# Kernel optimization log

Hardware: AMD Instinct MI355X
Metric: run time of the kernel (lower is better)

## Reference

```python
import jax, jax.numpy as jnp
import numpy as np

BUFFER_C = 1.25

def setup_inputs() -> dict:
    key = jax.random.key(0)
    k1, k2, k3 = jax.random.split(key, 3)
    T, D, E = 4096, 1024, 8
    x = jax.random.normal(k1, (T, D), dtype=jnp.float32)
    Wg = jax.random.normal(k2, (D, E), dtype=jnp.float32) / np.sqrt(D)
    bg = jnp.zeros((E,), dtype=jnp.float32)
    W = jax.random.normal(k3, (E, D, D), dtype=jnp.float32) / np.sqrt(D)
    b = jnp.zeros((E, D), dtype=jnp.float32)
    return {"x": x, "Wg": Wg, "bg": bg, "W": W, "b": b}


def reference(x, Wg, bg, W, b):
    # Top-1 (Switch-style) routing with capacity buffer, per-expert Linear,
    # prob-weighted combine, plus load-balancing aux loss.
    T, D = x.shape
    E = W.shape[0]
    capacity = int(BUFFER_C * T / E)

    logits = x @ Wg + bg                      # [T, E]
    probs = jax.nn.softmax(logits, axis=-1)   # [T, E]
    top_idx = jnp.argmax(probs, axis=-1)      # [T]
    top_prob = jnp.take_along_axis(probs, top_idx[:, None], axis=-1)[:, 0]

    onehot = jax.nn.one_hot(top_idx, E, dtype=x.dtype)       # [T, E]
    # 1-indexed position of each token within its expert's buffer
    pos = jnp.cumsum(onehot, axis=0) * onehot                # [T, E]
    dispatch = jnp.where((onehot > 0) & (pos <= capacity), 1.0, 0.0).astype(x.dtype)

    # dense dispatch/combine equivalent of the masked per-expert loop
    xe = jnp.einsum('te,td->etd', dispatch, x)               # [E, T, D]
    ye = jnp.einsum('etd,edf->etf', xe, W) + b[:, None, :]   # [E, T, D]
    y = jnp.einsum('te,etf->tf', dispatch, ye)               # [T, D] (0 for dropped)
    out = y * top_prob[:, None]

    # aux load-balance loss: E * sum_e f_e * P_e
    f = onehot.mean(axis=0)
    P = probs.mean(axis=0)
    aux_loss = E * jnp.sum(f * P)
    return out, aux_loss
```

## Files before the change

### kernel.cpp

```cpp
#include <hip/hip_runtime.h>
#include <hip/hip_bf16.h>
#include <cstdint>

#define T_TOK 4096
#define D_DIM 1024
#define E_EXP 8
#define CAP   640
#define MAXDROP 3456
#define MT    10
#define GBLK  1024

typedef __attribute__((ext_vector_type(8))) short short8;
typedef __attribute__((ext_vector_type(4))) float f32x4;

__device__ inline unsigned short f2bf(float f) {
    uint32_t u = __float_as_uint(f);
    u += 0x7fffu + ((u >> 16) & 1u);
    return (unsigned short)(u >> 16);
}

__device__ inline void dma16(const void* g, void* l) {
    __builtin_amdgcn_global_load_lds(
        (const __attribute__((address_space(1))) unsigned int*)g,
        (__attribute__((address_space(3))) unsigned int*)l, 16, 0, 0);
}

#define WB_TILE(e, nt, kt) ((((size_t)(e) * 16 + (nt)) * 16 + (kt)) * 4096)
#define XG_TILE(e, mt, kt) ((((size_t)(e) * MT + (mt)) * 16 + (kt)) * 4096)

__global__ __launch_bounds__(256) void prep_kernel(
    const float* __restrict__ x, const float* __restrict__ Wg,
    const float* __restrict__ bg, const float* __restrict__ W,
    unsigned short* __restrict__ Wb,
    int* __restrict__ top_idx, float* __restrict__ top_prob,
    float* __restrict__ blkpart)
{
    int bid = blockIdx.x;
    int tid = threadIdx.x;

    if (bid >= GBLK) {
        __shared__ unsigned short tile[64][66];
        int bid2 = bid - GBLK;
        int e  = bid2 >> 8;
        int kt = (bid2 >> 4) & 15;
        int nt = bid2 & 15;
        int k0 = kt * 64, n0 = nt * 64;
        const float* Wsrc = W + (size_t)e * D_DIM * D_DIM;
        #pragma unroll
        for (int p = 0; p < 4; p++) {
            int kk = p * 16 + (tid >> 4);
            int nn = (tid & 15) * 4;
            float4 v = *(const float4*)(Wsrc + (size_t)(k0 + kk) * D_DIM + n0 + nn);
            ushort4 u;
            u.x = f2bf(v.x); u.y = f2bf(v.y); u.z = f2bf(v.z); u.w = f2bf(v.w);
            *(ushort4*)&tile[kk][nn] = u;
        }
        __syncthreads();
        unsigned short* dst = Wb + WB_TILE(e, nt, kt);
        #pragma unroll
        for (int p = 0; p < 2; p++) {
            int c = tid + 256 * p;
            int g = c >> 6, n = c & 63;
            short8 v;
            #pragma unroll
            for (int z = 0; z < 8; z++) v[z] = (short)tile[g * 8 + z][n];
            *(short8*)&dst[(size_t)c * 8] = v;
        }
    } else {
        __shared__ float probs_sm[4][8];
        int wid  = tid >> 6;
        int lane = tid & 63;
        int t = bid * 4 + wid;

        const float* xr = x + (size_t)t * D_DIM;

        float acc[8];
        #pragma unroll
        for (int e = 0; e < 8; e++) acc[e] = 0.f;

        #pragma unroll
        for (int ii = 0; ii < 16; ii++) {
            int d = lane + 64 * ii;
            float xv = xr[d];
            const float4* wr = (const float4*)(Wg + (size_t)d * 8);
            float4 a = wr[0], bq = wr[1];
            acc[0] += xv * a.x;  acc[1] += xv * a.y;
            acc[2] += xv * a.z;  acc[3] += xv * a.w;
            acc[4] += xv * bq.x; acc[5] += xv * bq.y;
            acc[6] += xv * bq.z; acc[7] += xv * bq.w;
        }
        #pragma unroll
        for (int off = 32; off > 0; off >>= 1) {
            #pragma unroll
            for (int e = 0; e < 8; e++) acc[e] += __shfl_xor(acc[e], off, 64);
        }
        if (lane == 0) {
            float lg[8];
            #pragma unroll
            for (int e = 0; e < 8; e++) lg[e] = acc[e] + bg[e];
            float m = lg[0]; int am = 0;
            #pragma unroll
            for (int e = 1; e < 8; e++) { if (lg[e] > m) { m = lg[e]; am = e; } }
            float ex[8], s = 0.f;
            #pragma unroll
            for (int e = 0; e < 8; e++) { ex[e] = __expf(lg[e] - m); s += ex[e]; }
            float inv = 1.f / s;
            top_idx[t]  = am;
            top_prob[t] = ex[am] * inv;
            #pragma unroll
            for (int e = 0; e < 8; e++) probs_sm[wid][e] = 0.f;
            #pragma unroll
            for (int e = 0; e < 8; e++) probs_sm[wid][e] = ex[e] * inv;
        }
        __syncthreads();
        if (tid < 8) {
            float s = probs_sm[0][tid] + probs_sm[1][tid]
                    + probs_sm[2][tid] + probs_sm[3][tid];
            blkpart[(size_t)bid * 8 + tid] = s;
        }
    }
}

__global__ __launch_bounds__(1024) void scan_kernel(
    const int* __restrict__ top_idx,
    int* __restrict__ tok_list, int* __restrict__ cnt,
    const float* __restrict__ blkpart,
    float* __restrict__ out, float* __restrict__ out_aux)
{
    __shared__ int counts[64][8];
    __shared__ int excl[64][8];
    __shared__ int fulltot[8];
    __shared__ int droplist[MAXDROP];
    __shared__ int ndrop;
    __shared__ float wpart[16][8];

    int tid  = threadIdx.x;
    int wv   = tid >> 6;
    int lane = tid & 63;
    unsigned long long ltmask = (lane == 0) ? 0ull : ((~0ull) >> (64 - lane));

    if (tid == 0) ndrop = 0;

    float p[8];
    {
        const float4* bp = (const float4*)(blkpart + (size_t)tid * 8);
        float4 p0 = bp[0], p1 = bp[1];
        p[0] = p0.x; p[1] = p0.y; p[2] = p0.z; p[3] = p0.w;
        p[4] = p1.x; p[5] = p1.y; p[6] = p1.z; p[7] = p1.w;
    }

    int ecache[4];
    #pragma unroll
    for (int c = 0; c < 4; c++)
        ecache[c] = top_idx[(4 * wv + c) * 64 + lane];

    #pragma unroll
    for (int c = 0; c < 4; c++) {
        int chunk = 4 * wv + c;
        int e = ecache[c];
        #pragma unroll
        for (int q = 0; q < 8; q++) {
            unsigned long long mk = __ballot(e == q);
            int tot = __popcll(mk);
            if (lane == q) counts[chunk][q] = tot;
        }
    }
    __syncthreads();

    if (wv == 0) {
        #pragma unroll
        for (int q = 0; q < 8; q++) {
            int v = counts[lane][q];
            int orig = v;
            #pragma unroll
            for (int off = 1; off < 64; off <<= 1) {
                int n = __shfl_up(v, off, 64);
                if (lane >= off) v += n;
            }
            excl[lane][q] = v - orig;
            int total = __shfl(v, 63, 64);
            if (lane == 0) {
                fulltot[q] = total;
                cnt[q] = total < CAP ? total : CAP;
            }
        }
    }
    __syncthreads();

    #pragma unroll
    for (int c = 0; c < 4; c++) {
        int chunk = 4 * wv + c;
        int t = chunk * 64 + lane;
        int e = ecache[c];
        int pos = 0;
        #pragma unroll
        for (int q = 0; q < 8; q++) {
            unsigned long long mk = __ballot(e == q);
            if (e == q) pos = excl[chunk][q] + __popcll(mk & ltmask);
        }
        if (pos < CAP) {
            tok_list[e * CAP + pos] = t;
        } else {
            int di = atomicAdd(&ndrop, 1);
            droplist[di] = t;
        }
    }

    #pragma unroll
    for (int off = 32; off > 0; off >>= 1) {
        #pragma unroll
        for (int e = 0; e < 8; e++) p[e] += __shfl_xor(p[e], off, 64);
    }
    if (lane == 0) {
        #pragma unroll
        for (int e = 0; e < 8; e++) wpart[wv][e] = p[e];
    }
    __syncthreads();

    int nd = ndrop;
    int grp = tid >> 8;
    int col = (tid & 255) * 4;
    float4 z = {0.f, 0.f, 0.f, 0.f};
    for (int d = grp; d < nd; d += 4) {
        int row = droplist[d];
        *(float4*)&out[(size_t)row * D_DIM + col] = z;
    }

    if (tid == 0) {
        float s = 0.f;
        #pragma unroll
        for (int e = 0; e < 8; e++) {
            float Pe = 0.f;
            #pragma unroll
            for (int w = 0; w < 16; w++) Pe += wpart[w][e];
            s += ((float)fulltot[e] / (float)T_TOK) * (Pe / (float)T_TOK);
        }
        out_aux[0] = (float)E_EXP * s;
    }
}

__global__ __launch_bounds__(256) void gather_kernel(
    const float* __restrict__ x, const int* __restrict__ tok_list,
    const int* __restrict__ cnt, unsigned short* __restrict__ xg)
{
    int bid = blockIdx.x;
    int e   = bid / (MT * 16);
    int rem = bid % (MT * 16);
    int mt  = rem >> 4, kt = rem & 15;
    int count = cnt[e];
    int m0 = mt * 64;
    if (m0 >= count) return;

    int tid = threadIdx.x;
    const int* tl = tok_list + e * CAP;
    unsigned short* dst = xg + XG_TILE(e, mt, kt);

    #pragma unroll
    for (int p = 0; p < 2; p++) {
        int c = tid + 256 * p;
        int g = c >> 6, row = c & 63;
        int gm = m0 + row;
        int tok = tl[gm < count ? gm : count - 1];
        const float* src = x + (size_t)tok * D_DIM + kt * 64 + g * 8;
        float4 v0 = *(const float4*)(src);
        float4 v1 = *(const float4*)(src + 4);
        short8 v;
        v[0] = f2bf(v0.x); v[1] = f2bf(v0.y); v[2] = f2bf(v0.z); v[3] = f2bf(v0.w);
        v[4] = f2bf(v1.x); v[5] = f2bf(v1.y); v[6] = f2bf(v1.z); v[7] = f2bf(v1.w);
        *(short8*)&dst[(size_t)c * 8] = v;
    }
}

__device__ inline void stage_dma(const unsigned short* gAt, const unsigned short* gBt,
                                 unsigned short (*Ab)[64][8], unsigned short (*Bb)[64][8],
                                 int w, int lane)
{
    size_t lo = (size_t)lane * 8;
    dma16(gAt + (size_t)w * 512 + lo,       &Ab[w][0][0]);
    dma16(gAt + (size_t)(w + 4) * 512 + lo, &Ab[w + 4][0][0]);
    dma16(gBt + (size_t)w * 512 + lo,       &Bb[w][0][0]);
    dma16(gBt + (size_t)(w + 4) * 512 + lo, &Bb[w + 4][0][0]);
}

__global__ __launch_bounds__(256) void expert_gemm(
    const unsigned short* __restrict__ xg, const unsigned short* __restrict__ Wb,
    const float* __restrict__ bias,
    const int* __restrict__ tok_list, const int* __restrict__ cnt,
    const float* __restrict__ top_prob, float* __restrict__ out)
{
    int bid = blockIdx.x;
    int e   = bid / (MT * 16);
    int rem = bid % (MT * 16);
    int mt  = rem >> 4, nt = rem & 15;
    int count = cnt[e];
    int m0 = mt * 64;
    if (m0 >= count) return;
    int n0 = nt * 64;

    __shared__ unsigned short Ab[2][8][64][8];
    __shared__ unsigned short Bb[2][8][64][8];

    int tid  = threadIdx.x;
    int lane = tid & 63, w = tid >> 6;
    int quad = lane >> 4, l16 = lane & 15;
    int mw = (w >> 1) * 32, nw = (w & 1) * 32;

    const int* tl = tok_list + e * CAP;
    const unsigned short* gA0 = xg + XG_TILE(e, mt, 0);
    const unsigned short* gB0 = Wb + WB_TILE(e, nt, 0);

    f32x4 acc[2][2];
    #pragma unroll
    for (int i = 0; i < 2; i++)
        #pragma unroll
        for (int j = 0; j < 2; j++)
            acc[i][j] = (f32x4){0.f, 0.f, 0.f, 0.f};

    stage_dma(gA0, gB0, Ab[0], Bb[0], w, lane);

    int cur = 0;
    #pragma unroll 1
    for (int kt = 0; kt < 16; kt++) {
        __syncthreads();
        if (kt + 1 < 16)
            stage_dma(gA0 + (size_t)(kt + 1) * 4096, gB0 + (size_t)(kt + 1) * 4096,
                      Ab[cur ^ 1], Bb[cur ^ 1], w, lane);

        short8 af[2][2], bf[2][2];
        #pragma unroll
        for (int s = 0; s < 2; s++) {
            #pragma unroll
            for (int i = 0; i < 2; i++) {
                af[s][i] = *(const short8*)&Ab[cur][s * 4 + quad][mw + 16 * i + l16][0];
                bf[s][i] = *(const short8*)&Bb[cur][s * 4 + quad][nw + 16 * i + l16][0];
            }
        }
        #pragma unroll
        for (int s = 0; s < 2; s++)
            #pragma unroll
            for (int i = 0; i < 2; i++)
                #pragma unroll
                for (int j = 0; j < 2; j++)
                    acc[i][j] = __builtin_amdgcn_mfma_f32_16x16x32_bf16(
                        af[s][i], bf[s][j], acc[i][j], 0, 0, 0);
        cur ^= 1;
    }

    float bv[2];
    #pragma unroll
    for (int j = 0; j < 2; j++)
        bv[j] = bias[e * D_DIM + n0 + nw + 16 * j + l16];

    #pragma unroll
    for (int i = 0; i < 2; i++) {
        int rb = m0 + mw + 16 * i + quad * 4;
        #pragma unroll
        for (int r = 0; r < 4; r++) {
            int gm = rb + r;
            if (gm >= count) continue;
            int tok = tl[gm];
            float p = top_prob[tok];
            float* orow = out + (size_t)tok * D_DIM + n0 + nw + l16;
            #pragma unroll
            for (int j = 0; j < 2; j++)
                orow[16 * j] = (acc[i][j][r] + bv[j]) * p;
        }
    }
}

extern "C" void kernel_launch(void* const* d_in, const int* in_sizes, int n_in,
                              void* d_out, int out_size, void* d_ws, size_t ws_size,
                              hipStream_t stream) {
    const float* x  = (const float*)d_in[0];
    const float* Wg = (const float*)d_in[1];
    const float* bg = (const float*)d_in[2];
    const float* W  = (const float*)d_in[3];
    const float* b  = (const float*)d_in[4];
    float* out = (float*)d_out;

    char* ws = (char*)d_ws;
    unsigned short* Wb = (unsigned short*)(ws + 0);
    unsigned short* xg = (unsigned short*)(ws + 16777216);
    int*   top_idx  = (int*)(ws + 27262976);
    float* top_prob = (float*)(ws + 27279360);
    int*   tok_list = (int*)(ws + 27295744);
    int*   cnt      = (int*)(ws + 27316224);
    float* blkpart  = (float*)(ws + 27316256);

    hipLaunchKernelGGL(prep_kernel, dim3(GBLK + 2048), dim3(256), 0, stream,
                       x, Wg, bg, W, Wb, top_idx, top_prob, blkpart);
    hipLaunchKernelGGL(scan_kernel, dim3(1), dim3(1024), 0, stream,
                       top_idx, tok_list, cnt, blkpart, out, out + (size_t)T_TOK * D_DIM);
    hipLaunchKernelGGL(gather_kernel, dim3(E_EXP * MT * 16), dim3(256), 0, stream,
                       x, tok_list, cnt, xg);
    hipLaunchKernelGGL(expert_gemm, dim3(E_EXP * MT * 16), dim3(256), 0, stream,
                       xg, Wb, b, tok_list, cnt, top_prob, out);
}
```

Before: 143.3 us.

## Enlarge expert GEMM tiles to 128x128 with 4x4 MFMA per wave

The expert GEMM now uses 128x128 output tiles instead of 64x64. Each wave computes a 64x64 sub-tile with a 4x4 grid of MFMA accumulators, and K is staged in 32-wide slices over 32 iterations. This raises arithmetic intensity and cuts redundant A/B loads from global memory, but the grid drops to 320 blocks (fewer, when experts are underfilled) and register pressure rises. It also removes a redundant zeroing store in the router's shared probs buffer.

```diff
diff --git a/kernel.cpp b/kernel.cpp
--- a/kernel.cpp
+++ b/kernel.cpp
@@ -107,8 +107,6 @@
             float inv = 1.f / s;
             top_idx[t]  = am;
             top_prob[t] = ex[am] * inv;
-            #pragma unroll
-            for (int e = 0; e < 8; e++) probs_sm[wid][e] = 0.f;
             #pragma unroll
             for (int e = 0; e < 8; e++) probs_sm[wid][e] = ex[e] * inv;
         }
@@ -271,88 +269,84 @@
     }
 }
 
-__device__ inline void stage_dma(const unsigned short* gAt, const unsigned short* gBt,
-                                 unsigned short (*Ab)[64][8], unsigned short (*Bb)[64][8],
-                                 int w, int lane)
-{
-    size_t lo = (size_t)lane * 8;
-    dma16(gAt + (size_t)w * 512 + lo,       &Ab[w][0][0]);
-    dma16(gAt + (size_t)(w + 4) * 512 + lo, &Ab[w + 4][0][0]);
-    dma16(gBt + (size_t)w * 512 + lo,       &Bb[w][0][0]);
-    dma16(gBt + (size_t)(w + 4) * 512 + lo, &Bb[w + 4][0][0]);
-}
-
-__global__ __launch_bounds__(256) void expert_gemm(
+__global__ __launch_bounds__(256, 4) void expert_gemm(
     const unsigned short* __restrict__ xg, const unsigned short* __restrict__ Wb,
     const float* __restrict__ bias,
     const int* __restrict__ tok_list, const int* __restrict__ cnt,
     const float* __restrict__ top_prob, float* __restrict__ out)
 {
     int bid = blockIdx.x;
-    int e   = bid / (MT * 16);
-    int rem = bid % (MT * 16);
-    int mt  = rem >> 4, nt = rem & 15;
+    int e   = bid / 40;
+    int rem = bid % 40;
+    int mtb = rem >> 3, ntb = rem & 7;
     int count = cnt[e];
-    int m0 = mt * 64;
+    int m0 = mtb * 128;
     if (m0 >= count) return;
-    int n0 = nt * 64;
-
-    __shared__ unsigned short Ab[2][8][64][8];
-    __shared__ unsigned short Bb[2][8][64][8];
+    int n0 = ntb * 128;
+
+    __shared__ unsigned short Ab[2][4][128][8];
+    __shared__ unsigned short Bb[2][4][128][8];
 
     int tid  = threadIdx.x;
     int lane = tid & 63, w = tid >> 6;
     int quad = lane >> 4, l16 = lane & 15;
-    int mw = (w >> 1) * 32, nw = (w & 1) * 32;
+    int mw = (w >> 1) * 64, nw = (w & 1) * 64;
 
     const int* tl = tok_list + e * CAP;
-    const unsigned short* gA0 = xg + XG_TILE(e, mt, 0);
-    const unsigned short* gB0 = Wb + WB_TILE(e, nt, 0);
-
-    f32x4 acc[2][2];
-    #pragma unroll
-    for (int i = 0; i < 2; i++)
-        #pragma unroll
-        for (int j = 0; j < 2; j++)
+    const unsigned short* a0 = xg + XG_TILE(e, 2 * mtb,     0) + (size_t)w * 512 + (size_t)lane * 8;
+    const unsigned short* a1 = xg + XG_TILE(e, 2 * mtb + 1, 0) + (size_t)w * 512 + (size_t)lane * 8;
+    const unsigned short* b0 = Wb + WB_TILE(e, 2 * ntb,     0) + (size_t)w * 512 + (size_t)lane * 8;
+    const unsigned short* b1 = Wb + WB_TILE(e, 2 * ntb + 1, 0) + (size_t)w * 512 + (size_t)lane * 8;
+
+    f32x4 acc[4][4];
+    #pragma unroll
+    for (int i = 0; i < 4; i++)
+        #pragma unroll
+        for (int j = 0; j < 4; j++)
             acc[i][j] = (f32x4){0.f, 0.f, 0.f, 0.f};
 
-    stage_dma(gA0, gB0, Ab[0], Bb[0], w, lane);
+    #define STAGE(ks, buf) do {                                               \
+        size_t off = (size_t)((ks) >> 1) * 4096 + (size_t)((ks) & 1) * 2048;  \
+        dma16(a0 + off, &Ab[buf][w][0][0]);                                   \
+        dma16(a1 + off, &Ab[buf][w][64][0]);                                  \
+        dma16(b0 + off, &Bb[buf][w][0][0]);                                   \
+        dma16(b1 + off, &Bb[buf][w][64][0]);                                  \
+    } while (0)
+
+    STAGE(0, 0);
 
     int cur = 0;
     #pragma unroll 1
-    for (int kt = 0; kt < 16; kt++) {
+    for (int ks = 0; ks < 32; ks++) {
         __syncthreads();
-        if (kt + 1 < 16)
-            stage_dma(gA0 + (size_t)(kt + 1) * 4096, gB0 + (size_t)(kt + 1) * 4096,
-                      Ab[cur ^ 1], Bb[cur ^ 1], w, lane);
-
-        short8 af[2][2], bf[2][2];
-        #pragma unroll
-        for (int s = 0; s < 2; s++) {
-            #pragma unroll
-            for (int i = 0; i < 2; i++) {
-                af[s][i] = *(const short8*)&Ab[cur][s * 4 + quad][mw + 16 * i + l16][0];
-                bf[s][i] = *(const short8*)&Bb[cur][s * 4 + quad][nw + 16 * i + l16][0];
-            }
-        }
-        #pragma unroll
-        for (int s = 0; s < 2; s++)
-            #pragma unroll
-            for (int i = 0; i < 2; i++)
-                #pragma unroll
-                for (int j = 0; j < 2; j++)
-                    acc[i][j] = __builtin_amdgcn_mfma_f32_16x16x32_bf16(
-                        af[s][i], bf[s][j], acc[i][j], 0, 0, 0);
+        if (ks + 1 < 32)
+            STAGE(ks + 1, cur ^ 1);
+
+        short8 af[4], bf[4];
+        #pragma unroll
+        for (int i = 0; i < 4; i++)
+            af[i] = *(const short8*)&Ab[cur][quad][mw + 16 * i + l16][0];
+        #pragma unroll
+        for (int j = 0; j < 4; j++)
+            bf[j] = *(const short8*)&Bb[cur][quad][nw + 16 * j + l16][0];
+
+        #pragma unroll
+        for (int i = 0; i < 4; i++)
+            #pragma unroll
+            for (int j = 0; j < 4; j++)
+                acc[i][j] = __builtin_amdgcn_mfma_f32_16x16x32_bf16(
+                    af[i], bf[j], acc[i][j], 0, 0, 0);
         cur ^= 1;
     }
-
-    float bv[2];
-    #pragma unroll
-    for (int j = 0; j < 2; j++)
+    #undef STAGE
+
+    float bv[4];
+    #pragma unroll
+    for (int j = 0; j < 4; j++)
         bv[j] = bias[e * D_DIM + n0 + nw + 16 * j + l16];
 
     #pragma unroll
-    for (int i = 0; i < 2; i++) {
+    for (int i = 0; i < 4; i++) {
         int rb = m0 + mw + 16 * i + quad * 4;
         #pragma unroll
         for (int r = 0; r < 4; r++) {
@@ -362,7 +356,7 @@
             float p = top_prob[tok];
             float* orow = out + (size_t)tok * D_DIM + n0 + nw + l16;
             #pragma unroll
-            for (int j = 0; j < 2; j++)
+            for (int j = 0; j < 4; j++)
                 orow[16 * j] = (acc[i][j][r] + bv[j]) * p;
         }
     }
@@ -393,6 +387,6 @@
                        top_idx, tok_list, cnt, blkpart, out, out + (size_t)T_TOK * D_DIM);
     hipLaunchKernelGGL(gather_kernel, dim3(E_EXP * MT * 16), dim3(256), 0, stream,
                        x, tok_list, cnt, xg);
-    hipLaunchKernelGGL(expert_gemm, dim3(E_EXP * MT * 16), dim3(256), 0, stream,
+    hipLaunchKernelGGL(expert_gemm, dim3(E_EXP * 5 * 8), dim3(256), 0, stream,
                        xg, Wb, b, tok_list, cnt, top_prob, out);
 }
```

New measurement: 147.1 us. +2.6%, slower.
